# Performance work log

Hardware: AMD Instinct MI355X
Metric: run time of the kernel (lower is better)

Reference implementation:

```python
import jax, jax.numpy as jnp
import numpy as np

B, D_MODEL, D_HEAD, H, A = 1024, 1024, 64, 16, 4
EPS = 1e-6  # fast_transformers recurrent linear attention denominator eps


def setup_inputs() -> dict:
    key = jax.random.key(0)
    ks = jax.random.split(key, 24)
    s = 0.02
    n = jax.random.normal
    u = jax.random.uniform
    decay_u = u(ks[17], (H, D_HEAD), minval=0.001, maxval=0.2)
    return {
        "query": n(ks[0], (B, D_MODEL), jnp.float32),
        "key": n(ks[1], (B, D_MODEL), jnp.float32),
        "value": n(ks[2], (B, D_MODEL), jnp.float32),
        "matrix": n(ks[3], (B, H, D_HEAD, D_HEAD), jnp.float32) * 0.02,
        "normalizer": u(ks[4], (B, H, D_HEAD), jnp.float32) + 0.5,
        "Wq": n(ks[5], (H, D_HEAD, D_MODEL), jnp.float32) * s,
        "bq": jnp.zeros((H, D_HEAD), jnp.float32),
        "Wk": n(ks[6], (H, D_HEAD, D_MODEL), jnp.float32) * s,
        "bk": jnp.zeros((H, D_HEAD), jnp.float32),
        "Wv": n(ks[7], (H, D_HEAD, D_MODEL), jnp.float32) * s,
        "bv": jnp.zeros((H, D_HEAD), jnp.float32),
        "Wo": n(ks[8], (H, D_MODEL, D_HEAD), jnp.float32) * s,
        "bo": jnp.zeros((H, D_MODEL), jnp.float32),
        "We": n(ks[9], (H, D_MODEL), jnp.float32) * s,
        "be": jnp.zeros((H,), jnp.float32),
        "Ww": n(ks[10], (H, D_HEAD), jnp.float32) * s,
        "bw": jnp.zeros((H,), jnp.float32),
        "decay_logits": -jnp.log(1.0 / decay_u - 1.0),
    }


def reference(query, key, value, matrix, normalizer,
              Wq, bq, Wk, bk, Wv, bv, Wo, bo, We, be, Ww, bw, decay_logits):
    # ---- expert (head) routing: top-k over softmax of router logits ----
    logits = jnp.einsum('bm,hm->bh', query, We) + be          # [B,H]
    probs = jax.nn.softmax(logits, axis=-1)
    top_p, top_i = jax.lax.top_k(probs, A)                    # [B,A]
    top_logits = jnp.take_along_axis(logits, top_i, axis=-1)  # [B,A]

    # ---- banked head projections (compute all heads, gather active) ----
    def proj(x, W, b):
        return jnp.einsum('bm,hdm->bhd', x, W) + b            # [B,H,d]
    idx3 = top_i[:, :, None]
    q = jnp.take_along_axis(proj(query, Wq, bq), idx3, axis=1)  # [B,A,d]
    k = jnp.take_along_axis(proj(key, Wk, bk), idx3, axis=1)    # [B,A,d]
    v = jnp.take_along_axis(proj(value, Wv, bv), idx3, axis=1)  # [B,A,d]

    # ---- gather per-head recurrent state ----
    bidx = jnp.arange(B)[:, None]
    S = matrix[bidx, top_i]       # [B,A,d,d]
    Z = normalizer[bidx, top_i]   # [B,A,d]

    # ---- recurrent linear attention step (elu+1 feature map) ----
    phi_q = jax.nn.elu(q) + 1.0
    phi_k = jax.nn.elu(k) + 1.0
    dS = jnp.einsum('bad,bae->bade', phi_k, v)                # [B,A,d,d]
    S_new = S + dS
    Z_new = Z + phi_k
    num = jnp.einsum('bad,bade->bae', phi_q, S_new)
    den = jnp.einsum('bad,bad->ba', phi_q, Z_new) + EPS
    out = num / den[..., None]                                # [B,A,d]

    # ---- write gate + per-head decayed state update ----
    write_logits = top_logits + jnp.einsum('bad,bad->ba', out + q, Ww[top_i]) + bw[top_i]
    wp = jax.nn.sigmoid(write_logits)                         # [B,A]
    decay = jax.nn.sigmoid(decay_logits)[top_i]               # [B,A,d]
    Z_out = Z * (1.0 - wp[..., None] * decay) + wp[..., None] * phi_k
    S_out = S * (1.0 - wp[..., None, None] * decay[..., None]) + wp[..., None, None] * dS

    # ---- scatter updated states back into the full banks ----
    matrix_new = matrix.at[bidx, top_i].set(S_out)
    normalizer_new = normalizer.at[bidx, top_i].set(Z_out)

    # ---- merge heads: probability-weighted banked output projection ----
    # sum_a p_a * (Wo[i_a] @ out_a + bo[i_a]) == Wo applied to scatter of p*out
    full = jnp.zeros((B, H, D_HEAD), out.dtype).at[bidx, top_i].add(out * top_p[..., None])
    merged = jnp.einsum('bhe,hme->bm', full, Wo) + jnp.einsum('ba,bam->bm', top_p, bo[top_i])
    return merged, matrix_new, normalizer_new
```

## Files before the change

kernel.cpp:

```cpp
#include <hip/hip_runtime.h>
#include <hip/hip_bf16.h>

#define NB 1024
#define DM 1024
#define DH 64
#define NH 16
#define NA 4
#define FEPS 1e-6f
#define LP 68

__global__ __launch_bounds__(256) void k_route(
    const float* __restrict__ query,
    const float* __restrict__ We,
    const float* __restrict__ be,
    int* __restrict__ cnt,
    int* __restrict__ topi,
    float* __restrict__ topp,
    float* __restrict__ topl,
    int* __restrict__ slot,
    int* __restrict__ rows)
{
    int b = blockIdx.x, t = threadIdx.x;
    __shared__ float qs[DM];
    __shared__ float lg[NH];
    __shared__ int   sti[NA];
    __shared__ float stp[NA], stl[NA];
    ((float4*)qs)[t] = ((const float4*)(query + (size_t)b*DM))[t];
    __syncthreads();
    int h = t >> 4, l = t & 15;
    const float* w = We + h*DM;
    float p = 0.f;
    for (int j = l; j < DM; j += 16) p += qs[j]*w[j];
    #pragma unroll
    for (int d = 8; d > 0; d >>= 1) p += __shfl_down(p, d, 16);
    if (l == 0) lg[h] = p + be[h];
    __syncthreads();
    if (t == 0) {
        float mx = lg[0];
        for (int i = 1; i < NH; i++) mx = fmaxf(mx, lg[i]);
        float s = 0.f, e[NH];
        for (int i = 0; i < NH; i++) { e[i] = expf(lg[i]-mx); s += e[i]; }
        float inv = 1.f/s;
        unsigned used = 0;
        for (int a = 0; a < NA; a++) {
            int bi = -1; float bv = -1e30f;
            for (int i = 0; i < NH; i++)
                if (!((used>>i)&1u) && lg[i] > bv) { bv = lg[i]; bi = i; }
            used |= 1u << bi;
            sti[a] = bi; stp[a] = e[bi]*inv; stl[a] = lg[bi];
        }
    }
    __syncthreads();
    if (t < NA) {
        int hh = sti[t];
        topi[b*NA+t] = hh; topp[b*NA+t] = stp[t]; topl[b*NA+t] = stl[t];
        int pos = atomicAdd(&cnt[hh], 1);
        rows[hh*NB + pos] = b*NA + t;
    }
    if (t < NH) {
        int sl = -1;
        #pragma unroll
        for (int a = 0; a < NA; a++) if (sti[a] == t) sl = a;
        slot[b*NH + t] = sl;
    }
}

__global__ __launch_bounds__(256) void k_proj(
    const float* __restrict__ Xq, const float* __restrict__ Xk, const float* __restrict__ Xv,
    const float* __restrict__ Wq, const float* __restrict__ Wk, const float* __restrict__ Wv,
    const float* __restrict__ bq, const float* __restrict__ bk, const float* __restrict__ bv,
    const int* __restrict__ cnt, const int* __restrict__ rows,
    float* __restrict__ qb, float* __restrict__ kb, float* __restrict__ vb)
{
    int h = blockIdx.x, c = blockIdx.y, pz = blockIdx.z;
    int n = cnt[h];
    int r0 = c*64;
    if (r0 >= n) return;
    int nr = min(64, n - r0);
    const float* X    = pz==0 ? Xq : (pz==1 ? Xk : Xv);
    const float* W    = (pz==0 ? Wq : (pz==1 ? Wk : Wv)) + (size_t)h*DH*DM;
    const float* bias = (pz==0 ? bq : (pz==1 ? bk : bv)) + h*DH;
    float* outp = pz==0 ? qb : (pz==1 ? kb : vb);

    __shared__ float As[64*LP];
    __shared__ float Bs[64*LP];
    __shared__ int codes[64];
    int t = threadIdx.x;
    if (t < 64) codes[t] = rows[h*NB + r0 + min(t, nr-1)];
    __syncthreads();
    int tx = t & 15, ty = t >> 4;
    float acc[4][4] = {};
    int lr = t >> 2, k0 = (t & 3)*16;
    const float* srcA0 = X + (size_t)(codes[lr] >> 2)*DM + k0;
    const float* srcB0 = W + (size_t)lr*DM + k0;
    for (int kt = 0; kt < DM; kt += 64) {
        #pragma unroll
        for (int j = 0; j < 4; j++) {
            float4 fa = ((const float4*)(srcA0 + kt))[j];
            float4 fb = ((const float4*)(srcB0 + kt))[j];
            int kk = k0 + j*4;
            As[(kk+0)*LP + lr] = fa.x; As[(kk+1)*LP + lr] = fa.y;
            As[(kk+2)*LP + lr] = fa.z; As[(kk+3)*LP + lr] = fa.w;
            Bs[(kk+0)*LP + lr] = fb.x; Bs[(kk+1)*LP + lr] = fb.y;
            Bs[(kk+2)*LP + lr] = fb.z; Bs[(kk+3)*LP + lr] = fb.w;
        }
        __syncthreads();
        #pragma unroll 8
        for (int k = 0; k < 64; k++) {
            float4 a4 = *(const float4*)(As + k*LP + ty*4);
            float4 b4 = *(const float4*)(Bs + k*LP + tx*4);
            float a0[4] = {a4.x, a4.y, a4.z, a4.w};
            float b0[4] = {b4.x, b4.y, b4.z, b4.w};
            #pragma unroll
            for (int i=0;i<4;i++)
                #pragma unroll
                for (int j=0;j<4;j++) acc[i][j] += a0[i]*b0[j];
        }
        __syncthreads();
    }
    #pragma unroll
    for (int i = 0; i < 4; i++) {
        int r = ty*4+i;
        if (r < nr) {
            int code = codes[r];
            #pragma unroll
            for (int j = 0; j < 4; j++)
                outp[code*DH + tx*4+j] = acc[i][j] + bias[tx*4+j];
        }
    }
}

__global__ __launch_bounds__(256) void k_update(
    const float* __restrict__ matrix,
    const float* __restrict__ normalizer,
    const float* __restrict__ Ww, const float* __restrict__ bw,
    const float* __restrict__ dlog,
    const int* __restrict__ slot, const float* __restrict__ topl,
    const float* __restrict__ qb, const float* __restrict__ kb,
    const float* __restrict__ vb, float* __restrict__ ob,
    float* __restrict__ om, float* __restrict__ on)
{
    int bh = blockIdx.x, t = threadIdx.x;
    const float* S = matrix + (size_t)bh*(DH*DH);
    float* So = om + (size_t)bh*(DH*DH);
    int sl = slot[bh];
    if (sl < 0) {
        #pragma unroll
        for (int j = 0; j < 4; j++) {
            int i4 = t + 256*j;
            ((float4*)So)[i4] = ((const float4*)S)[i4];
        }
        if (t < DH)
            on[(size_t)bh*DH + t] = normalizer[(size_t)bh*DH + t];
        return;
    }
    int b = bh >> 4, h = bh & 15;
    int code = b*NA + sl;
    __shared__ float st[DH*DH];
    __shared__ float pq[DH], pk[DH], vv[DH], qv[DH], Zs[DH];
    __shared__ float part[256];
    __shared__ float fd[DH], gd[DH];
    __shared__ float scal[4];
    if (t < DH) {
        float qq = qb[code*DH + t]; qv[t] = qq;
        float kk = kb[code*DH + t];
        pq[t] = qq > 0.f ? qq + 1.f : expf(qq);
        pk[t] = kk > 0.f ? kk + 1.f : expf(kk);
        vv[t] = vb[code*DH + t];
        Zs[t] = normalizer[(size_t)bh*DH + t];
    }
    #pragma unroll
    for (int j = 0; j < 4; j++)
        ((float4*)st)[t + 256*j] = ((const float4*)S)[t + 256*j];
    __syncthreads();
    {
        int e = t & 63, dg = t >> 6;
        float s = 0.f;
        #pragma unroll
        for (int d = 0; d < 16; d++) s += pq[dg*16 + d] * st[(dg*16+d)*DH + e];
        part[t] = s;
    }
    if (t < 64) {
        float r1 = pq[t]*pk[t];
        float r2 = pq[t]*(Zs[t]+pk[t]);
        #pragma unroll
        for (int d = 32; d > 0; d >>= 1) {
            r1 += __shfl_down(r1, d, 64);
            r2 += __shfl_down(r2, d, 64);
        }
        if (t == 0) { scal[0] = r1; scal[1] = r2 + FEPS; }
    }
    __syncthreads();
    float pqk = scal[0], den = scal[1];
    if (t < 64) {
        float cs = part[t] + part[64+t] + part[128+t] + part[192+t];
        float o = (cs + pqk*vv[t]) / den;
        ob[code*DH + t] = o;
        float r3 = (o + qv[t]) * Ww[h*DH + t];
        #pragma unroll
        for (int d = 32; d > 0; d >>= 1) r3 += __shfl_down(r3, d, 64);
        if (t == 0) {
            float wl = topl[code] + r3 + bw[h];
            scal[2] = 1.f/(1.f + expf(-wl));
        }
    }
    __syncthreads();
    float wp = scal[2];
    if (t < 64) {
        float dec = 1.f/(1.f + expf(-dlog[h*DH + t]));
        float f1 = 1.f - wp*dec;
        fd[t] = f1;
        gd[t] = wp*pk[t];
        on[(size_t)bh*DH + t] = Zs[t]*f1 + wp*pk[t];
    }
    __syncthreads();
    #pragma unroll
    for (int j = 0; j < 4; j++) {
        int i4 = t + 256*j;
        int d = i4 >> 4, e0 = (i4 & 15)*4;
        float4 f = ((const float4*)st)[i4];
        float F = fd[d], G = gd[d];
        float4 u = { f.x*F + G*vv[e0],   f.y*F + G*vv[e0+1],
                     f.z*F + G*vv[e0+2], f.w*F + G*vv[e0+3] };
        ((float4*)So)[i4] = u;
    }
}

__global__ __launch_bounds__(256) void k_mergemm(
    const float* __restrict__ Wo,
    const int* __restrict__ cnt, const int* __restrict__ rows,
    const float* __restrict__ topp, const float* __restrict__ ob,
    float* __restrict__ contrib)
{
    int h = blockIdx.x, rt = blockIdx.y, mt = blockIdx.z;
    int n = cnt[h];
    int r0 = rt*64;
    if (r0 >= n) return;
    int nr = min(64, n - r0);

    __shared__ float As[64*LP];
    __shared__ float Bs[64*LP];
    __shared__ int   codes[64];
    __shared__ float scl[64];
    int t = threadIdx.x;
    if (t < 64) {
        int c = rows[h*NB + r0 + min(t, nr-1)];
        codes[t] = c;
        scl[t] = topp[c];
    }
    __syncthreads();

    int lr = t >> 2, e0 = (t & 3)*16;
    {
        const float* srcA = ob + (size_t)codes[lr]*DH + e0;
        float sc = scl[lr];
        const float* srcB = Wo + (size_t)h*DM*DH + (size_t)(mt*64 + lr)*DH + e0;
        #pragma unroll
        for (int j = 0; j < 4; j++) {
            float4 fa = ((const float4*)srcA)[j];
            float4 fb = ((const float4*)srcB)[j];
            int ee = e0 + j*4;
            As[(ee+0)*LP + lr] = fa.x*sc; As[(ee+1)*LP + lr] = fa.y*sc;
            As[(ee+2)*LP + lr] = fa.z*sc; As[(ee+3)*LP + lr] = fa.w*sc;
            Bs[(ee+0)*LP + lr] = fb.x;    Bs[(ee+1)*LP + lr] = fb.y;
            Bs[(ee+2)*LP + lr] = fb.z;    Bs[(ee+3)*LP + lr] = fb.w;
        }
    }
    __syncthreads();

    int tx = t & 15, ty = t >> 4;
    float acc[4][4] = {};
    #pragma unroll 8
    for (int k = 0; k < 64; k++) {
        float4 a4 = *(const float4*)(As + k*LP + ty*4);
        float4 b4 = *(const float4*)(Bs + k*LP + tx*4);
        float a0[4] = {a4.x, a4.y, a4.z, a4.w};
        float b0[4] = {b4.x, b4.y, b4.z, b4.w};
        #pragma unroll
        for (int i=0;i<4;i++)
            #pragma unroll
            for (int j=0;j<4;j++) acc[i][j] += a0[i]*b0[j];
    }

    int mbase = mt*64 + tx*4;
    #pragma unroll
    for (int i = 0; i < 4; i++) {
        int r = ty*4 + i;
        if (r < nr) {
            float4 u = { acc[i][0], acc[i][1], acc[i][2], acc[i][3] };
            *(float4*)(contrib + (size_t)codes[r]*DM + mbase) = u;
        }
    }
}

__global__ __launch_bounds__(256) void k_finalize(
    const int* __restrict__ topi, const float* __restrict__ topp,
    const float* __restrict__ bo, const float* __restrict__ contrib,
    float* __restrict__ merged)
{
    int b = blockIdx.x, t = threadIdx.x;
    __shared__ float tp[NA];
    __shared__ int   hh[NA];
    if (t < NA) { tp[t] = topp[b*NA+t]; hh[t] = topi[b*NA+t]; }
    __syncthreads();
    float ax = 0.f, ay = 0.f, az = 0.f, aw = 0.f;
    #pragma unroll
    for (int a = 0; a < NA; a++) {
        float4 cv = ((const float4*)(contrib + (size_t)(b*NA + a)*DM))[t];
        float4 w  = ((const float4*)(bo + (size_t)hh[a]*DM))[t];
        float p = tp[a];
        ax += cv.x + p*w.x; ay += cv.y + p*w.y;
        az += cv.z + p*w.z; aw += cv.w + p*w.w;
    }
    float4 u = { ax, ay, az, aw };
    ((float4*)merged)[(size_t)b*(DM/4) + t] = u;
}

extern "C" void kernel_launch(void* const* d_in, const int* in_sizes, int n_in,
                              void* d_out, int out_size, void* d_ws, size_t ws_size,
                              hipStream_t stream)
{
    const float* query  = (const float*)d_in[0];
    const float* key    = (const float*)d_in[1];
    const float* value  = (const float*)d_in[2];
    const float* matrix = (const float*)d_in[3];
    const float* normal = (const float*)d_in[4];
    const float* Wq = (const float*)d_in[5];
    const float* bq = (const float*)d_in[6];
    const float* Wk = (const float*)d_in[7];
    const float* bk = (const float*)d_in[8];
    const float* Wv = (const float*)d_in[9];
    const float* bv = (const float*)d_in[10];
    const float* Wo = (const float*)d_in[11];
    const float* bo = (const float*)d_in[12];
    const float* We = (const float*)d_in[13];
    const float* be = (const float*)d_in[14];
    const float* Ww = (const float*)d_in[15];
    const float* bw = (const float*)d_in[16];
    const float* dlog = (const float*)d_in[17];

    float* ws = (float*)d_ws;
    int*   cnt  = (int*)ws;
    int*   topi = (int*)(ws + 16);
    float* topp = ws + 16 + 4096;
    float* topl = topp + 4096;
    int*   slot = (int*)(topl + 4096);
    int*   rows = slot + 16384;
    float* qb = (float*)(rows + 16384);
    float* kb = qb + 262144;
    float* vb = kb + 262144;
    float* ob = vb + 262144;
    float* contrib = ob + 262144;

    float* out_merged = (float*)d_out;
    float* out_matrix = out_merged + (size_t)NB*DM;
    float* out_norm   = out_matrix + (size_t)NB*NH*DH*DH;

    hipMemsetAsync(cnt, 0, 16*sizeof(int), stream);
    k_route<<<NB, 256, 0, stream>>>(query, We, be, cnt, topi, topp, topl, slot, rows);
    k_proj<<<dim3(NH, NB/64, 3), 256, 0, stream>>>(query, key, value, Wq, Wk, Wv,
                                                   bq, bk, bv, cnt, rows, qb, kb, vb);
    k_update<<<NB*NH, 256, 0, stream>>>(matrix, normal, Ww, bw, dlog, slot, topl,
                                        qb, kb, vb, ob, out_matrix, out_norm);
    k_mergemm<<<dim3(NH, NB/64, DM/64), 256, 0, stream>>>(Wo, cnt, rows, topp, ob,
                                                          contrib);
    k_finalize<<<NB, 256, 0, stream>>>(topi, topp, bo, contrib, out_merged);
}
```

Before: 628.8 us.

## Use bf16 MFMA for head projection and merge GEMMs

Replaces the FP32 scalar outer-product GEMM loops in the projection and merge kernels with bf16 MFMA 16x16x32 instructions. Inputs are converted to bf16 with round-to-nearest-even while staging into shared memory, in a fragment-friendly layout. This targets the FP32 FMA throughput bound of the GEMMs, at the cost of reduced input precision (bf16) and less coalesced scalar output stores.

```diff
diff --git a/kernel.cpp b/kernel.cpp
--- a/kernel.cpp
+++ b/kernel.cpp
@@ -7,7 +7,18 @@
 #define NH 16
 #define NA 4
 #define FEPS 1e-6f
-#define LP 68
+
+typedef __attribute__((ext_vector_type(8))) short s16x8;
+typedef __attribute__((ext_vector_type(4))) float f32x4;
+
+__device__ __forceinline__ unsigned short f2bf(float f) {
+    unsigned u = __builtin_bit_cast(unsigned, f);
+    u += 0x7FFFu + ((u >> 16) & 1u);
+    return (unsigned short)(u >> 16);
+}
+__device__ __forceinline__ unsigned pk2(float x, float y) {
+    return (unsigned)f2bf(x) | ((unsigned)f2bf(y) << 16);
+}
 
 __global__ __launch_bounds__(256) void k_route(
     const float* __restrict__ query,
@@ -82,50 +93,67 @@
     const float* bias = (pz==0 ? bq : (pz==1 ? bk : bv)) + h*DH;
     float* outp = pz==0 ? qb : (pz==1 ? kb : vb);
 
-    __shared__ float As[64*LP];
-    __shared__ float Bs[64*LP];
+    __shared__ __align__(16) unsigned short Af[4*2*64*8];
+    __shared__ __align__(16) unsigned short Bf[4*2*64*8];
     __shared__ int codes[64];
     int t = threadIdx.x;
     if (t < 64) codes[t] = rows[h*NB + r0 + min(t, nr-1)];
     __syncthreads();
-    int tx = t & 15, ty = t >> 4;
-    float acc[4][4] = {};
-    int lr = t >> 2, k0 = (t & 3)*16;
-    const float* srcA0 = X + (size_t)(codes[lr] >> 2)*DM + k0;
-    const float* srcB0 = W + (size_t)lr*DM + k0;
+
+    int lane = t & 63, wv = t >> 6;
+    int lr = t >> 2;
+    int ks = (t & 3) * 16;
+    int sA = ks >> 5;
+    int g0 = (ks >> 3) & 3;
+    int grp = lr >> 4;
+    int dst0 = ((grp*2 + sA)*64 + (lr & 15) + g0*16) * 8;
+    int dst1 = ((grp*2 + sA)*64 + (lr & 15) + (g0+1)*16) * 8;
+    const float* srcA = X + (size_t)(codes[lr] >> 2)*DM + ks;
+    const float* srcB = W + (size_t)lr*DM + ks;
+
+    f32x4 acc[4] = {};
     for (int kt = 0; kt < DM; kt += 64) {
-        #pragma unroll
-        for (int j = 0; j < 4; j++) {
-            float4 fa = ((const float4*)(srcA0 + kt))[j];
-            float4 fb = ((const float4*)(srcB0 + kt))[j];
-            int kk = k0 + j*4;
-            As[(kk+0)*LP + lr] = fa.x; As[(kk+1)*LP + lr] = fa.y;
-            As[(kk+2)*LP + lr] = fa.z; As[(kk+3)*LP + lr] = fa.w;
-            Bs[(kk+0)*LP + lr] = fb.x; Bs[(kk+1)*LP + lr] = fb.y;
-            Bs[(kk+2)*LP + lr] = fb.z; Bs[(kk+3)*LP + lr] = fb.w;
-        }
+        float4 a0 = ((const float4*)(srcA + kt))[0];
+        float4 a1 = ((const float4*)(srcA + kt))[1];
+        float4 a2 = ((const float4*)(srcA + kt))[2];
+        float4 a3 = ((const float4*)(srcA + kt))[3];
+        float4 b0 = ((const float4*)(srcB + kt))[0];
+        float4 b1 = ((const float4*)(srcB + kt))[1];
+        float4 b2 = ((const float4*)(srcB + kt))[2];
+        float4 b3 = ((const float4*)(srcB + kt))[3];
+        uint4 pA0 = { pk2(a0.x,a0.y), pk2(a0.z,a0.w), pk2(a1.x,a1.y), pk2(a1.z,a1.w) };
+        uint4 pA1 = { pk2(a2.x,a2.y), pk2(a2.z,a2.w), pk2(a3.x,a3.y), pk2(a3.z,a3.w) };
+        uint4 pB0 = { pk2(b0.x,b0.y), pk2(b0.z,b0.w), pk2(b1.x,b1.y), pk2(b1.z,b1.w) };
+        uint4 pB1 = { pk2(b2.x,b2.y), pk2(b2.z,b2.w), pk2(b3.x,b3.y), pk2(b3.z,b3.w) };
+        *(uint4*)(Af + dst0) = pA0;
+        *(uint4*)(Af + dst1) = pA1;
+        *(uint4*)(Bf + dst0) = pB0;
+        *(uint4*)(Bf + dst1) = pB1;
         __syncthreads();
-        #pragma unroll 8
-        for (int k = 0; k < 64; k++) {
-            float4 a4 = *(const float4*)(As + k*LP + ty*4);
-            float4 b4 = *(const float4*)(Bs + k*LP + tx*4);
-            float a0[4] = {a4.x, a4.y, a4.z, a4.w};
-            float b0[4] = {b4.x, b4.y, b4.z, b4.w};
+        #pragma unroll
+        for (int s = 0; s < 2; s++) {
+            s16x8 av = *(const s16x8*)(Af + ((wv*2 + s)*64 + lane)*8);
             #pragma unroll
-            for (int i=0;i<4;i++)
-                #pragma unroll
-                for (int j=0;j<4;j++) acc[i][j] += a0[i]*b0[j];
+            for (int mt = 0; mt < 4; mt++) {
+                s16x8 bv = *(const s16x8*)(Bf + ((mt*2 + s)*64 + lane)*8);
+                acc[mt] = __builtin_amdgcn_mfma_f32_16x16x32_bf16(av, bv, acc[mt], 0, 0, 0);
+            }
         }
         __syncthreads();
     }
-    #pragma unroll
-    for (int i = 0; i < 4; i++) {
-        int r = ty*4+i;
+
+    int rbase = wv*16 + (lane >> 4)*4;
+    #pragma unroll
+    for (int reg = 0; reg < 4; reg++) {
+        int r = rbase + reg;
         if (r < nr) {
             int code = codes[r];
+            float* dst = outp + (size_t)code*DH;
             #pragma unroll
-            for (int j = 0; j < 4; j++)
-                outp[code*DH + tx*4+j] = acc[i][j] + bias[tx*4+j];
+            for (int mt = 0; mt < 4; mt++) {
+                int m = mt*16 + (lane & 15);
+                dst[m] = acc[mt][reg] + bias[m];
+            }
         }
     }
 }
@@ -232,63 +260,75 @@
     const float* __restrict__ topp, const float* __restrict__ ob,
     float* __restrict__ contrib)
 {
-    int h = blockIdx.x, rt = blockIdx.y, mt = blockIdx.z;
+    int h = blockIdx.x, rt = blockIdx.y, mtile = blockIdx.z;
     int n = cnt[h];
     int r0 = rt*64;
     if (r0 >= n) return;
     int nr = min(64, n - r0);
 
-    __shared__ float As[64*LP];
-    __shared__ float Bs[64*LP];
-    __shared__ int   codes[64];
-    __shared__ float scl[64];
+    __shared__ __align__(16) unsigned short Af[4*2*64*8];
+    __shared__ __align__(16) unsigned short Bf[4*2*64*8];
+    __shared__ int codes[64];
     int t = threadIdx.x;
-    if (t < 64) {
-        int c = rows[h*NB + r0 + min(t, nr-1)];
-        codes[t] = c;
-        scl[t] = topp[c];
-    }
-    __syncthreads();
-
-    int lr = t >> 2, e0 = (t & 3)*16;
+    if (t < 64) codes[t] = rows[h*NB + r0 + min(t, nr-1)];
+    __syncthreads();
+
+    int lane = t & 63, wv = t >> 6;
+    int lr = t >> 2;
+    int es = (t & 3) * 16;
+    int sA = es >> 5;
+    int g0 = (es >> 3) & 3;
+    int grp = lr >> 4;
+    int dst0 = ((grp*2 + sA)*64 + (lr & 15) + g0*16) * 8;
+    int dst1 = ((grp*2 + sA)*64 + (lr & 15) + (g0+1)*16) * 8;
+
     {
-        const float* srcA = ob + (size_t)codes[lr]*DH + e0;
-        float sc = scl[lr];
-        const float* srcB = Wo + (size_t)h*DM*DH + (size_t)(mt*64 + lr)*DH + e0;
-        #pragma unroll
-        for (int j = 0; j < 4; j++) {
-            float4 fa = ((const float4*)srcA)[j];
-            float4 fb = ((const float4*)srcB)[j];
-            int ee = e0 + j*4;
-            As[(ee+0)*LP + lr] = fa.x*sc; As[(ee+1)*LP + lr] = fa.y*sc;
-            As[(ee+2)*LP + lr] = fa.z*sc; As[(ee+3)*LP + lr] = fa.w*sc;
-            Bs[(ee+0)*LP + lr] = fb.x;    Bs[(ee+1)*LP + lr] = fb.y;
-            Bs[(ee+2)*LP + lr] = fb.z;    Bs[(ee+3)*LP + lr] = fb.w;
-        }
-    }
-    __syncthreads();
-
-    int tx = t & 15, ty = t >> 4;
-    float acc[4][4] = {};
-    #pragma unroll 8
-    for (int k = 0; k < 64; k++) {
-        float4 a4 = *(const float4*)(As + k*LP + ty*4);
-        float4 b4 = *(const float4*)(Bs + k*LP + tx*4);
-        float a0[4] = {a4.x, a4.y, a4.z, a4.w};
-        float b0[4] = {b4.x, b4.y, b4.z, b4.w};
-        #pragma unroll
-        for (int i=0;i<4;i++)
+        int codeA = codes[lr];
+        float sc = topp[codeA];
+        const float* srcA = ob + (size_t)codeA*DH + es;
+        const float* srcB = Wo + (size_t)h*DM*DH + (size_t)(mtile*64 + lr)*DH + es;
+        float4 a0 = ((const float4*)srcA)[0];
+        float4 a1 = ((const float4*)srcA)[1];
+        float4 a2 = ((const float4*)srcA)[2];
+        float4 a3 = ((const float4*)srcA)[3];
+        float4 b0 = ((const float4*)srcB)[0];
+        float4 b1 = ((const float4*)srcB)[1];
+        float4 b2 = ((const float4*)srcB)[2];
+        float4 b3 = ((const float4*)srcB)[3];
+        uint4 pA0 = { pk2(a0.x*sc,a0.y*sc), pk2(a0.z*sc,a0.w*sc),
+                      pk2(a1.x*sc,a1.y*sc), pk2(a1.z*sc,a1.w*sc) };
+        uint4 pA1 = { pk2(a2.x*sc,a2.y*sc), pk2(a2.z*sc,a2.w*sc),
+                      pk2(a3.x*sc,a3.y*sc), pk2(a3.z*sc,a3.w*sc) };
+        uint4 pB0 = { pk2(b0.x,b0.y), pk2(b0.z,b0.w), pk2(b1.x,b1.y), pk2(b1.z,b1.w) };
+        uint4 pB1 = { pk2(b2.x,b2.y), pk2(b2.z,b2.w), pk2(b3.x,b3.y), pk2(b3.z,b3.w) };
+        *(uint4*)(Af + dst0) = pA0;
+        *(uint4*)(Af + dst1) = pA1;
+        *(uint4*)(Bf + dst0) = pB0;
+        *(uint4*)(Bf + dst1) = pB1;
+    }
+    __syncthreads();
+
+    f32x4 acc[4] = {};
+    #pragma unroll
+    for (int s = 0; s < 2; s++) {
+        s16x8 av = *(const s16x8*)(Af + ((wv*2 + s)*64 + lane)*8);
+        #pragma unroll
+        for (int mt = 0; mt < 4; mt++) {
+            s16x8 bv = *(const s16x8*)(Bf + ((mt*2 + s)*64 + lane)*8);
+            acc[mt] = __builtin_amdgcn_mfma_f32_16x16x32_bf16(av, bv, acc[mt], 0, 0, 0);
+        }
+    }
+
+    int rbase = wv*16 + (lane >> 4)*4;
+    int mbase = mtile*64 + (lane & 15);
+    #pragma unroll
+    for (int reg = 0; reg < 4; reg++) {
+        int r = rbase + reg;
+        if (r < nr) {
+            float* dst = contrib + (size_t)codes[r]*DM + mbase;
             #pragma unroll
-            for (int j=0;j<4;j++) acc[i][j] += a0[i]*b0[j];
-    }
-
-    int mbase = mt*64 + tx*4;
-    #pragma unroll
-    for (int i = 0; i < 4; i++) {
-        int r = ty*4 + i;
-        if (r < nr) {
-            float4 u = { acc[i][0], acc[i][1], acc[i][2], acc[i][3] };
-            *(float4*)(contrib + (size_t)codes[r]*DM + mbase) = u;
+            for (int mt = 0; mt < 4; mt++)
+                dst[mt*16] = acc[mt][reg];
         }
     }
 }
```

After: 572.8 us. -8.9%, faster.
